# Performance work log

Hardware: AMD Instinct MI355X
Metric: run time of the kernel (lower is better)

## Reference

```python
import jax, jax.numpy as jnp
import numpy as np

# ---- configuration mirrored from init_kwargs ----
NUM_TREES = 8
NUM_NODES = 5
C = 16          # in_channels
B, H, W = 8, 224, 224
SEED = 0
NEG = -1e30     # maxplus semiring zero (avoid -inf for fp16/bf16 safety)


def make_forest():
    """Random recursive trees: node 0 is the root, parent[i] < i."""
    rng = np.random.default_rng(SEED)
    parents = []
    for _ in range(NUM_TREES):
        p = [-1] + [int(rng.integers(0, i)) for i in range(1, NUM_NODES)]
        parents.append(p)
    return parents


def excl_prefix_max(v):
    """Strict 2D prefix max: out[h,w] = max over h'<h, w'<w of v[h',w'].
    Semiring 'cumulative sum' (maxplus add = max) with exclusive shift."""
    c = jax.lax.cummax(jax.lax.cummax(v, axis=2), axis=3)
    c = c[:, :, :-1, :-1]
    return jnp.pad(c, ((0, 0), (0, 0), (1, 0), (1, 0)), constant_values=NEG)


def setup_inputs() -> dict:
    key = jax.random.key(0)
    kx, ka = jax.random.split(key)
    x = jax.random.normal(kx, (B, C, H, W), dtype=jnp.float32)
    alphas = jax.random.normal(ka, (NUM_TREES, NUM_NODES, C), dtype=jnp.float32)
    return {"x": x, "alphas": alphas}


def reference(x, alphas):
    parents = make_forest()  # static structure (seed-fixed)
    # valuate: map to log domain for the maxplus semiring
    xv = jnp.log1p(jax.nn.relu(x))  # [B, C, H, W]

    outs = []
    for t in range(NUM_TREES):
        par = parents[t]
        acc = [None] * NUM_NODES   # maxplus-product (= +) of children prefix maxes
        root_val = None
        # bottom-up over nodes (parent index < child index)
        for i in range(NUM_NODES - 1, -1, -1):
            # maxplus scaling by alpha: alpha + x
            v = xv + alphas[t, i][None, :, None, None]
            if acc[i] is not None:
                v = v + acc[i]          # semiring product with children
            if i > 0:
                s = excl_prefix_max(v)  # semiring cumulative over quadrant
                p = par[i]
                acc[p] = s if acc[p] is None else acc[p] + s
            else:
                root_val = v
        # root aggregation: maxplus sum over all pixels -> [B, C]
        outs.append(jnp.max(root_val, axis=(2, 3)))
    res = jnp.stack(outs, axis=1)  # [B, NUM_TREES, C]
    # devaluate: back from log domain
    return jnp.expm1(res)
```

## Files before the change

kernel.cpp:

```cpp
#include <hip/hip_runtime.h>
#include <stdint.h>

#define NTREES 8
#define NNODES 5
#define CC 16
#define BB 8
#define HH 224
#define WW 224
#define NBAND 56

struct Forest { int par[NTREES * NNODES]; };
struct Cls { int v[NTREES]; };

namespace nprng {

struct Pcg {
  __uint128_t state, inc;
  int has_uint32;
  uint32_t uinteger;
};

static inline __uint128_t pcg_mult() {
  return (((__uint128_t)0x2360ED051FC65DA4ULL) << 64) | 0x4385DF649FCCF645ULL;
}

static inline void pcg_step(Pcg& s) { s.state = s.state * pcg_mult() + s.inc; }

static inline uint64_t pcg_next64(Pcg& s) {
  pcg_step(s);
  uint64_t xored = (uint64_t)(s.state >> 64) ^ (uint64_t)s.state;
  unsigned rot = (unsigned)(s.state >> 122);
  return (xored >> rot) | (xored << ((64u - rot) & 63u));
}

static inline uint32_t pcg_next32(Pcg& s) {
  if (s.has_uint32) { s.has_uint32 = 0; return s.uinteger; }
  uint64_t n = pcg_next64(s);
  s.has_uint32 = 1;
  s.uinteger = (uint32_t)(n >> 32);
  return (uint32_t)n;
}

static inline uint32_t lemire32(Pcg& s, uint32_t rng) {
  const uint32_t rng_excl = rng + 1u;
  uint64_t m = (uint64_t)pcg_next32(s) * (uint64_t)rng_excl;
  uint32_t leftover = (uint32_t)m;
  if (leftover < rng_excl) {
    const uint32_t threshold = (uint32_t)((0xFFFFFFFFu - rng) % rng_excl);
    while (leftover < threshold) {
      m = (uint64_t)pcg_next32(s) * (uint64_t)rng_excl;
      leftover = (uint32_t)m;
    }
  }
  return (uint32_t)(m >> 32);
}

static void make_forest(Forest& f) {
  const uint32_t INIT_A = 0x43b0d7e5u, MULT_A = 0x931e8875u;
  const uint32_t INIT_B = 0x8b51f9ddu, MULT_B = 0x58f38dedu;
  const uint32_t MIX_L  = 0xca01f9ddu, MIX_R  = 0x4973f715u;
  uint32_t pool[4];
  uint32_t hc = INIT_A;
  auto hashmix = [&](uint32_t v) -> uint32_t {
    v ^= hc; hc *= MULT_A; v *= hc; v ^= v >> 16; return v;
  };
  auto mix = [&](uint32_t x, uint32_t y) -> uint32_t {
    uint32_t r = MIX_L * x - MIX_R * y; r ^= r >> 16; return r;
  };
  pool[0] = hashmix(0u);
  for (int i = 1; i < 4; ++i) pool[i] = hashmix(0u);
  for (int is = 0; is < 4; ++is)
    for (int id = 0; id < 4; ++id)
      if (is != id) pool[id] = mix(pool[id], hashmix(pool[is]));
  uint32_t st32[8];
  uint32_t hb = INIT_B;
  for (int i = 0; i < 8; ++i) {
    uint32_t dv = pool[i & 3];
    dv ^= hb; hb *= MULT_B; dv *= hb; dv ^= dv >> 16;
    st32[i] = dv;
  }
  uint64_t w64[4];
  for (int i = 0; i < 4; ++i)
    w64[i] = (uint64_t)st32[2 * i] | ((uint64_t)st32[2 * i + 1] << 32);

  __uint128_t initstate = (((__uint128_t)w64[0]) << 64) | w64[1];
  __uint128_t initseq   = (((__uint128_t)w64[2]) << 64) | w64[3];
  Pcg s;
  s.state = 0; s.inc = (initseq << 1) | 1;
  pcg_step(s);
  s.state += initstate;
  pcg_step(s);
  s.has_uint32 = 0; s.uinteger = 0;

  for (int t = 0; t < NTREES; ++t) {
    f.par[t * NNODES + 0] = -1;
    for (int i = 1; i < NNODES; ++i) {
      uint32_t rng = (uint32_t)(i - 1);
      f.par[t * NNODES + i] = (rng == 0) ? 0 : (int)lemire32(s, rng);
    }
  }
}

}

static int classify_tree(const int* p) {
  int nch[NNODES] = {0, 0, 0, 0, 0};
  for (int i = 1; i < NNODES; ++i) nch[p[i]]++;
  int internals[3], nI = 0;
  for (int i = 1; i <= 3; ++i) if (nch[i] > 0) internals[nI++] = i;
  if (nI == 0) return 1;
  if (nI == 1) {
    int m = nch[internals[0]];
    return m == 1 ? 2 : (m == 2 ? 3 : 4);
  }
  if (nI == 2) {
    int i = internals[0], j = internals[1];
    if (p[j] == i) {
      if (nch[j] == 2) return 9;
      return (nch[i] - 1 == 1) ? 7 : 6;
    }
    return 5;
  }
  return 8;
}

template <int CL> struct TC;
template <> struct TC<1> { static constexpr int H1=0,E1L=0,H2=0,E2L=0,H3=0,RL=4,R1=0,R2=0,R3=0; };
template <> struct TC<2> { static constexpr int H1=1,E1L=1,H2=0,E2L=0,H3=0,RL=2,R1=1,R2=0,R3=0; };
template <> struct TC<3> { static constexpr int H1=1,E1L=2,H2=0,E2L=0,H3=0,RL=1,R1=1,R2=0,R3=0; };
template <> struct TC<4> { static constexpr int H1=1,E1L=3,H2=0,E2L=0,H3=0,RL=0,R1=1,R2=0,R3=0; };
template <> struct TC<5> { static constexpr int H1=1,E1L=1,H2=0,E2L=0,H3=0,RL=0,R1=2,R2=0,R3=0; };
template <> struct TC<6> { static constexpr int H1=1,E1L=1,H2=1,E2L=0,H3=0,RL=1,R1=0,R2=1,R3=0; };
template <> struct TC<7> { static constexpr int H1=1,E1L=1,H2=1,E2L=1,H3=0,RL=0,R1=0,R2=1,R3=0; };
template <> struct TC<8> { static constexpr int H1=1,E1L=1,H2=1,E2L=0,H3=1,RL=0,R1=0,R2=0,R3=1; };
template <> struct TC<9> { static constexpr int H1=1,E1L=2,H2=1,E2L=0,H3=0,RL=0,R1=0,R2=1,R3=0; };

__device__ __forceinline__ float wshr1(float t) {
  int r = __builtin_amdgcn_update_dpp(
      0, __builtin_bit_cast(int, t), 0x138, 0xf, 0xf, true);
  return __builtin_bit_cast(float, r);
}

#define S4STAGE(MODS) \
  "v_max_f32_dpp %0, %0, %0 " MODS "\n\t" \
  "v_max_f32_dpp %1, %1, %1 " MODS "\n\t" \
  "v_max_f32_dpp %2, %2, %2 " MODS "\n\t" \
  "v_max_f32_dpp %3, %3, %3 " MODS "\n\t"

#define SCAN4(a, b, c, d)                                     \
  asm volatile(                                               \
      "s_nop 1\n\t"                                           \
      S4STAGE("row_shr:1 row_mask:0xf bank_mask:0xf")         \
      S4STAGE("row_shr:2 row_mask:0xf bank_mask:0xf")         \
      S4STAGE("row_shr:4 row_mask:0xf bank_mask:0xf")         \
      S4STAGE("row_shr:8 row_mask:0xf bank_mask:0xf")         \
      S4STAGE("row_bcast:15 row_mask:0xa bank_mask:0xf")      \
      S4STAGE("row_bcast:31 row_mask:0xc bank_mask:0xf")      \
      "s_nop 1"                                               \
      : "+v"(a), "+v"(b), "+v"(c), "+v"(d))

#define MUL4(d, s) { (d).x *= (s).x; (d).y *= (s).y; (d).z *= (s).z; (d).w *= (s).w; }
#define MAX4(d, s) { (d).x = fmaxf((d).x,(s).x); (d).y = fmaxf((d).y,(s).y); \
                     (d).z = fmaxf((d).z,(s).z); (d).w = fmaxf((d).w,(s).w); }

template <int E>
__device__ __forceinline__ void powmul(float4& v, const float4& s) {
  if constexpr (E == 4) {
    float4 t = s; MUL4(t, t); MUL4(t, t); MUL4(v, t);
  } else {
    if constexpr (E >= 1) MUL4(v, s);
    if constexpr (E >= 2) MUL4(v, s);
    if constexpr (E >= 3) MUL4(v, s);
  }
}

__device__ __forceinline__ void scan_pass(const float4 v[4], float4 S[4],
                                          const float4& carry) {
  float l1a = fmaxf(v[0].x, v[0].y), l2a = fmaxf(l1a, v[0].z), qa = fmaxf(l2a, v[0].w);
  float l1b = fmaxf(v[1].x, v[1].y), l2b = fmaxf(l1b, v[1].z), qb = fmaxf(l2b, v[1].w);
  float l1c = fmaxf(v[2].x, v[2].y), l2c = fmaxf(l1c, v[2].z), qc = fmaxf(l2c, v[2].w);
  float l1d = fmaxf(v[3].x, v[3].y), l2d = fmaxf(l1d, v[3].z), qd = fmaxf(l2d, v[3].w);
  SCAN4(qa, qb, qc, qd);
  float4 run = carry;
  {
    float e = wshr1(qa);
    run.x = fmaxf(run.x, e);
    run.y = fmaxf(run.y, fmaxf(e, v[0].x));
    run.z = fmaxf(run.z, fmaxf(e, l1a));
    run.w = fmaxf(run.w, fmaxf(e, l2a));
    S[0] = run;
  }
  {
    float e = wshr1(qb);
    run.x = fmaxf(run.x, e);
    run.y = fmaxf(run.y, fmaxf(e, v[1].x));
    run.z = fmaxf(run.z, fmaxf(e, l1b));
    run.w = fmaxf(run.w, fmaxf(e, l2b));
    S[1] = run;
  }
  {
    float e = wshr1(qc);
    run.x = fmaxf(run.x, e);
    run.y = fmaxf(run.y, fmaxf(e, v[2].x));
    run.z = fmaxf(run.z, fmaxf(e, l1c));
    run.w = fmaxf(run.w, fmaxf(e, l2c));
    S[2] = run;
  }
  {
    float e = wshr1(qd);
    run.x = fmaxf(run.x, e);
    run.y = fmaxf(run.y, fmaxf(e, v[3].x));
    run.z = fmaxf(run.z, fmaxf(e, l1d));
    run.w = fmaxf(run.w, fmaxf(e, l2d));
    S[3] = run;
  }
}

template <int CL>
__device__ __forceinline__ void run_tree(const float* __restrict__ cp,
                                         float mask, float asum,
                                         float* __restrict__ outp, int lane) {
  using F = TC<CL>;
  const float4 z4 = make_float4(0.f, 0.f, 0.f, 0.f);
  float4 cL = z4, c1 = z4, c2 = z4, c3 = z4, racc = z4;

  float4 X[4];
#pragma unroll
  for (int u = 0; u < 4; ++u) X[u] = *(const float4*)(cp + u * WW);

#pragma unroll 1
  for (int band = 0; band < NBAND; ++band) {
    const int nb = (band + 1 < NBAND) ? band + 1 : NBAND - 1;
    float4 T[4];
#pragma unroll
    for (int u = 0; u < 4; ++u)
      T[u] = *(const float4*)(cp + (size_t)(nb * 4 + u) * WW);

    float4 fv[4];
#pragma unroll
    for (int u = 0; u < 4; ++u) {
      const float4 xr = X[u];
      fv[u].x = fmaf(fmaxf(xr.x, 0.f), mask, mask);
      fv[u].y = fmaf(fmaxf(xr.y, 0.f), mask, mask);
      fv[u].z = fmaf(fmaxf(xr.z, 0.f), mask, mask);
      fv[u].w = fmaf(fmaxf(xr.w, 0.f), mask, mask);
    }

    float4 SL[4], S1[4], S2[4], S3[4];

    scan_pass(fv, SL, cL);

    if constexpr (F::H1) {
      float4 v[4];
#pragma unroll
      for (int u = 0; u < 4; ++u) {
        v[u] = fv[u];
        powmul<F::E1L>(v[u], (u == 0) ? cL : SL[u - 1]);
      }
      scan_pass(v, S1, c1);
    }

    if constexpr (F::H2) {
      float4 v[4];
#pragma unroll
      for (int u = 0; u < 4; ++u) {
        v[u] = fv[u];
        if constexpr (F::E2L > 0) powmul<F::E2L>(v[u], (u == 0) ? cL : SL[u - 1]);
        { float4 s = (u == 0) ? c1 : S1[u - 1]; MUL4(v[u], s); }
      }
      scan_pass(v, S2, c2);
    }

    if constexpr (F::H3) {
      float4 v[4];
#pragma unroll
      for (int u = 0; u < 4; ++u) {
        v[u] = fv[u];
        { float4 s = (u == 0) ? c2 : S2[u - 1]; MUL4(v[u], s); }
      }
      scan_pass(v, S3, c3);
    }

#pragma unroll
    for (int u = 0; u < 4; ++u) {
      float4 r = fv[u];
      if constexpr (F::RL > 0) powmul<F::RL>(r, (u == 0) ? cL : SL[u - 1]);
      if constexpr (F::R1 > 0) powmul<F::R1>(r, (u == 0) ? c1 : S1[u - 1]);
      if constexpr (F::R2 > 0) powmul<F::R2>(r, (u == 0) ? c2 : S2[u - 1]);
      if constexpr (F::R3 > 0) powmul<F::R3>(r, (u == 0) ? c3 : S3[u - 1]);
      MAX4(racc, r);
    }

    cL = SL[3];
    if constexpr (F::H1) c1 = S1[3];
    if constexpr (F::H2) c2 = S2[3];
    if constexpr (F::H3) c3 = S3[3];

#pragma unroll
    for (int u = 0; u < 4; ++u) X[u] = T[u];
  }

  float m = fmaxf(fmaxf(racc.x, racc.y), fmaxf(racc.z, racc.w));
#pragma unroll
  for (int d = 1; d < 64; d <<= 1) m = fmaxf(m, __shfl_xor(m, d));
  if (lane == 0) *outp = expf(asum) * m - 1.f;
}

__global__ __launch_bounds__(64) void fis_kernel(const float* __restrict__ x,
                                                 const float* __restrict__ alphas,
                                                 float* __restrict__ out,
                                                 Cls cls) {
  const int lane = threadIdx.x;
  const int blk  = blockIdx.x;
  const int t    = blk >> 7;
  const int bc   = blk & 127;
  const int c    = bc & (CC - 1);
  const int b    = bc >> 4;

  const float* __restrict__ xp = x + (size_t)bc * (HH * WW);

  float asum = 0.f;
#pragma unroll
  for (int i = 0; i < NNODES; ++i) asum += alphas[(t * NNODES + i) * CC + c];

  const int   w0   = lane * 4;
  const float mask = (w0 < WW) ? 1.0f : 0.0f;
  const float* __restrict__ cp = xp + ((w0 < WW) ? w0 : (WW - 4));
  float* outp = out + ((size_t)b * NTREES + t) * CC + c;

  switch (cls.v[t]) {
    case 1: run_tree<1>(cp, mask, asum, outp, lane); break;
    case 2: run_tree<2>(cp, mask, asum, outp, lane); break;
    case 3: run_tree<3>(cp, mask, asum, outp, lane); break;
    case 4: run_tree<4>(cp, mask, asum, outp, lane); break;
    case 5: run_tree<5>(cp, mask, asum, outp, lane); break;
    case 6: run_tree<6>(cp, mask, asum, outp, lane); break;
    case 7: run_tree<7>(cp, mask, asum, outp, lane); break;
    case 8: run_tree<8>(cp, mask, asum, outp, lane); break;
    case 9: run_tree<9>(cp, mask, asum, outp, lane); break;
    default: break;
  }
}

extern "C" void kernel_launch(void* const* d_in, const int* in_sizes, int n_in,
                              void* d_out, int out_size, void* d_ws, size_t ws_size,
                              hipStream_t stream) {
  const float* x      = (const float*)d_in[0];
  const float* alphas = (const float*)d_in[1];
  float* out          = (float*)d_out;

  Forest f;
  nprng::make_forest(f);

  Cls cls;
  for (int t = 0; t < NTREES; ++t)
    cls.v[t] = classify_tree(&f.par[t * NNODES]);

  dim3 grid(BB * CC * NTREES);
  dim3 block(64);
  hipLaunchKernelGGL(fis_kernel, grid, block, 0, stream, x, alphas, out, cls);
}
```

Baseline: 100.3 us.

## Software-pipeline tree depth levels across bands to batch DPP scans

Restructures the per-band loop so each tree depth level works on a band lagged by one per level. All level scans then go into a single batched DPP asm block of up to 16 independent chains instead of several dependent 4-wide scans. This is meant to hide DPP latency and cut s_nop and serialization overhead per band. In exchange it keeps more live registers (delayed fv copies, previous-band scan state) and runs a few extra drain iterations with a zeroed mask.

```diff
diff --git a/kernel.cpp b/kernel.cpp
--- a/kernel.cpp
+++ b/kernel.cpp
@@ -141,23 +141,34 @@
   return __builtin_bit_cast(float, r);
 }
 
-#define S4STAGE(MODS) \
-  "v_max_f32_dpp %0, %0, %0 " MODS "\n\t" \
-  "v_max_f32_dpp %1, %1, %1 " MODS "\n\t" \
-  "v_max_f32_dpp %2, %2, %2 " MODS "\n\t" \
-  "v_max_f32_dpp %3, %3, %3 " MODS "\n\t"
-
-#define SCAN4(a, b, c, d)                                     \
-  asm volatile(                                               \
-      "s_nop 1\n\t"                                           \
-      S4STAGE("row_shr:1 row_mask:0xf bank_mask:0xf")         \
-      S4STAGE("row_shr:2 row_mask:0xf bank_mask:0xf")         \
-      S4STAGE("row_shr:4 row_mask:0xf bank_mask:0xf")         \
-      S4STAGE("row_shr:8 row_mask:0xf bank_mask:0xf")         \
-      S4STAGE("row_bcast:15 row_mask:0xa bank_mask:0xf")      \
-      S4STAGE("row_bcast:31 row_mask:0xc bank_mask:0xf")      \
-      "s_nop 1"                                               \
-      : "+v"(a), "+v"(b), "+v"(c), "+v"(d))
+#define DPP_S1  "row_shr:1 row_mask:0xf bank_mask:0xf"
+#define DPP_S2  "row_shr:2 row_mask:0xf bank_mask:0xf"
+#define DPP_S4  "row_shr:4 row_mask:0xf bank_mask:0xf"
+#define DPP_S8  "row_shr:8 row_mask:0xf bank_mask:0xf"
+#define DPP_B15 "row_bcast:15 row_mask:0xa bank_mask:0xf"
+#define DPP_B31 "row_bcast:31 row_mask:0xc bank_mask:0xf"
+
+#define OPROW(n, M) "v_max_f32_dpp %" #n ", %" #n ", %" #n " " M "\n\t"
+
+#define OPS4(M)  OPROW(0,M) OPROW(1,M) OPROW(2,M) OPROW(3,M)
+#define OPS8(M)  OPS4(M)  OPROW(4,M) OPROW(5,M) OPROW(6,M) OPROW(7,M)
+#define OPS12(M) OPS8(M)  OPROW(8,M) OPROW(9,M) OPROW(10,M) OPROW(11,M)
+#define OPS16(M) OPS12(M) OPROW(12,M) OPROW(13,M) OPROW(14,M) OPROW(15,M)
+
+#define SCANBODY(OPS) \
+  "s_nop 1\n\t" OPS(DPP_S1) OPS(DPP_S2) OPS(DPP_S4) OPS(DPP_S8) \
+  OPS(DPP_B15) OPS(DPP_B31) "s_nop 1"
+
+#define SCAN4Q(q)  asm volatile(SCANBODY(OPS4)  : "+v"((q)[0]), "+v"((q)[1]), "+v"((q)[2]), "+v"((q)[3]))
+#define SCAN8Q(q)  asm volatile(SCANBODY(OPS8)  : "+v"((q)[0]), "+v"((q)[1]), "+v"((q)[2]), "+v"((q)[3]), \
+                                                  "+v"((q)[4]), "+v"((q)[5]), "+v"((q)[6]), "+v"((q)[7]))
+#define SCAN12Q(q) asm volatile(SCANBODY(OPS12) : "+v"((q)[0]), "+v"((q)[1]), "+v"((q)[2]), "+v"((q)[3]), \
+                                                  "+v"((q)[4]), "+v"((q)[5]), "+v"((q)[6]), "+v"((q)[7]), \
+                                                  "+v"((q)[8]), "+v"((q)[9]), "+v"((q)[10]), "+v"((q)[11]))
+#define SCAN16Q(q) asm volatile(SCANBODY(OPS16) : "+v"((q)[0]), "+v"((q)[1]), "+v"((q)[2]), "+v"((q)[3]), \
+                                                  "+v"((q)[4]), "+v"((q)[5]), "+v"((q)[6]), "+v"((q)[7]), \
+                                                  "+v"((q)[8]), "+v"((q)[9]), "+v"((q)[10]), "+v"((q)[11]), \
+                                                  "+v"((q)[12]), "+v"((q)[13]), "+v"((q)[14]), "+v"((q)[15]))
 
 #define MUL4(d, s) { (d).x *= (s).x; (d).y *= (s).y; (d).z *= (s).z; (d).w *= (s).w; }
 #define MAX4(d, s) { (d).x = fmaxf((d).x,(s).x); (d).y = fmaxf((d).y,(s).y); \
@@ -174,45 +185,34 @@
   }
 }
 
-__device__ __forceinline__ void scan_pass(const float4 v[4], float4 S[4],
-                                          const float4& carry) {
-  float l1a = fmaxf(v[0].x, v[0].y), l2a = fmaxf(l1a, v[0].z), qa = fmaxf(l2a, v[0].w);
-  float l1b = fmaxf(v[1].x, v[1].y), l2b = fmaxf(l1b, v[1].z), qb = fmaxf(l2b, v[1].w);
-  float l1c = fmaxf(v[2].x, v[2].y), l2c = fmaxf(l1c, v[2].z), qc = fmaxf(l2c, v[2].w);
-  float l1d = fmaxf(v[3].x, v[3].y), l2d = fmaxf(l1d, v[3].z), qd = fmaxf(l2d, v[3].w);
-  SCAN4(qa, qb, qc, qd);
-  float4 run = carry;
-  {
-    float e = wshr1(qa);
+__device__ __forceinline__ float4 srcat(const float4 S[4], const float4& tail, int u) {
+  return (u == 0) ? tail : S[u - 1];
+}
+
+struct LocB { float x0[4], l1[4], l2[4]; };
+
+__device__ __forceinline__ void mk_q(const float4 v[4], LocB& L, float* q) {
+#pragma unroll
+  for (int u = 0; u < 4; ++u) {
+    L.x0[u] = v[u].x;
+    L.l1[u] = fmaxf(v[u].x, v[u].y);
+    L.l2[u] = fmaxf(L.l1[u], v[u].z);
+    q[u]    = fmaxf(L.l2[u], v[u].w);
+  }
+}
+
+__device__ __forceinline__ void run_update(const LocB& L, const float* q,
+                                           float4 S[4], float4& tail) {
+  tail = S[3];
+  float4 run = tail;
+#pragma unroll
+  for (int u = 0; u < 4; ++u) {
+    float e = wshr1(q[u]);
     run.x = fmaxf(run.x, e);
-    run.y = fmaxf(run.y, fmaxf(e, v[0].x));
-    run.z = fmaxf(run.z, fmaxf(e, l1a));
-    run.w = fmaxf(run.w, fmaxf(e, l2a));
-    S[0] = run;
-  }
-  {
-    float e = wshr1(qb);
-    run.x = fmaxf(run.x, e);
-    run.y = fmaxf(run.y, fmaxf(e, v[1].x));
-    run.z = fmaxf(run.z, fmaxf(e, l1b));
-    run.w = fmaxf(run.w, fmaxf(e, l2b));
-    S[1] = run;
-  }
-  {
-    float e = wshr1(qc);
-    run.x = fmaxf(run.x, e);
-    run.y = fmaxf(run.y, fmaxf(e, v[2].x));
-    run.z = fmaxf(run.z, fmaxf(e, l1c));
-    run.w = fmaxf(run.w, fmaxf(e, l2c));
-    S[2] = run;
-  }
-  {
-    float e = wshr1(qd);
-    run.x = fmaxf(run.x, e);
-    run.y = fmaxf(run.y, fmaxf(e, v[3].x));
-    run.z = fmaxf(run.z, fmaxf(e, l1d));
-    run.w = fmaxf(run.w, fmaxf(e, l2d));
-    S[3] = run;
+    run.y = fmaxf(run.y, fmaxf(e, L.x0[u]));
+    run.z = fmaxf(run.z, fmaxf(e, L.l1[u]));
+    run.w = fmaxf(run.w, fmaxf(e, L.l2[u]));
+    S[u] = run;
   }
 }
 
@@ -221,81 +221,129 @@
                                          float mask, float asum,
                                          float* __restrict__ outp, int lane) {
   using F = TC<CL>;
+  constexpr int D = 1 + F::H1 + F::H2 + F::H3;
+  constexpr bool NEEDM1 = (F::H2 != 0) && (F::E2L > 0 || F::RL > 0);
   const float4 z4 = make_float4(0.f, 0.f, 0.f, 0.f);
-  float4 cL = z4, c1 = z4, c2 = z4, c3 = z4, racc = z4;
+
+  float4 SL[4] = {z4, z4, z4, z4}, S1[4] = {z4, z4, z4, z4};
+  float4 S2[4] = {z4, z4, z4, z4}, S3[4] = {z4, z4, z4, z4};
+  float4 SLm1[4] = {z4, z4, z4, z4};
+  float4 tailL = z4, tail1 = z4, tail2 = z4, tail3 = z4, tailLm1 = z4;
+  float4 fv1[4] = {z4, z4, z4, z4}, fv2[4] = {z4, z4, z4, z4},
+         fv3[4] = {z4, z4, z4, z4};
+  float4 racc = z4;
 
   float4 X[4];
 #pragma unroll
   for (int u = 0; u < 4; ++u) X[u] = *(const float4*)(cp + u * WW);
 
 #pragma unroll 1
-  for (int band = 0; band < NBAND; ++band) {
-    const int nb = (band + 1 < NBAND) ? band + 1 : NBAND - 1;
+  for (int i = 0; i < NBAND + D - 1; ++i) {
+    const int nb = (i + 1 < NBAND) ? (i + 1) : (NBAND - 1);
     float4 T[4];
 #pragma unroll
     for (int u = 0; u < 4; ++u)
       T[u] = *(const float4*)(cp + (size_t)(nb * 4 + u) * WW);
 
-    float4 fv[4];
+    const float bm = (i < NBAND) ? mask : 0.f;
+    float4 fv0[4];
 #pragma unroll
     for (int u = 0; u < 4; ++u) {
-      const float4 xr = X[u];
-      fv[u].x = fmaf(fmaxf(xr.x, 0.f), mask, mask);
-      fv[u].y = fmaf(fmaxf(xr.y, 0.f), mask, mask);
-      fv[u].z = fmaf(fmaxf(xr.z, 0.f), mask, mask);
-      fv[u].w = fmaf(fmaxf(xr.w, 0.f), mask, mask);
-    }
-
-    float4 SL[4], S1[4], S2[4], S3[4];
-
-    scan_pass(fv, SL, cL);
-
+      fv0[u].x = fmaf(fmaxf(X[u].x, 0.f), bm, bm);
+      fv0[u].y = fmaf(fmaxf(X[u].y, 0.f), bm, bm);
+      fv0[u].z = fmaf(fmaxf(X[u].z, 0.f), bm, bm);
+      fv0[u].w = fmaf(fmaxf(X[u].w, 0.f), bm, bm);
+    }
+
+    LocB loL, lo1, lo2, lo3;
+    float q[16];
+    mk_q(fv0, loL, q + 0);
     if constexpr (F::H1) {
       float4 v[4];
 #pragma unroll
       for (int u = 0; u < 4; ++u) {
-        v[u] = fv[u];
-        powmul<F::E1L>(v[u], (u == 0) ? cL : SL[u - 1]);
+        v[u] = fv1[u];
+        powmul<F::E1L>(v[u], srcat(SL, tailL, u));
       }
-      scan_pass(v, S1, c1);
-    }
-
+      mk_q(v, lo1, q + 4);
+    }
     if constexpr (F::H2) {
       float4 v[4];
 #pragma unroll
       for (int u = 0; u < 4; ++u) {
-        v[u] = fv[u];
-        if constexpr (F::E2L > 0) powmul<F::E2L>(v[u], (u == 0) ? cL : SL[u - 1]);
-        { float4 s = (u == 0) ? c1 : S1[u - 1]; MUL4(v[u], s); }
+        v[u] = fv2[u];
+        if constexpr (F::E2L > 0) powmul<F::E2L>(v[u], srcat(SLm1, tailLm1, u));
+        float4 s = srcat(S1, tail1, u);
+        MUL4(v[u], s);
       }
-      scan_pass(v, S2, c2);
-    }
-
+      mk_q(v, lo2, q + 8);
+    }
     if constexpr (F::H3) {
       float4 v[4];
 #pragma unroll
       for (int u = 0; u < 4; ++u) {
-        v[u] = fv[u];
-        { float4 s = (u == 0) ? c2 : S2[u - 1]; MUL4(v[u], s); }
+        v[u] = fv3[u];
+        float4 s = srcat(S2, tail2, u);
+        MUL4(v[u], s);
       }
-      scan_pass(v, S3, c3);
-    }
-
-#pragma unroll
-    for (int u = 0; u < 4; ++u) {
-      float4 r = fv[u];
-      if constexpr (F::RL > 0) powmul<F::RL>(r, (u == 0) ? cL : SL[u - 1]);
-      if constexpr (F::R1 > 0) powmul<F::R1>(r, (u == 0) ? c1 : S1[u - 1]);
-      if constexpr (F::R2 > 0) powmul<F::R2>(r, (u == 0) ? c2 : S2[u - 1]);
-      if constexpr (F::R3 > 0) powmul<F::R3>(r, (u == 0) ? c3 : S3[u - 1]);
-      MAX4(racc, r);
-    }
-
-    cL = SL[3];
-    if constexpr (F::H1) c1 = S1[3];
-    if constexpr (F::H2) c2 = S2[3];
-    if constexpr (F::H3) c3 = S3[3];
-
+      mk_q(v, lo3, q + 12);
+    }
+
+    if constexpr (D == 1)      { SCAN4Q(q); }
+    else if constexpr (D == 2) { SCAN8Q(q); }
+    else if constexpr (D == 3) { SCAN12Q(q); }
+    else                       { SCAN16Q(q); }
+
+    if constexpr (F::H3) run_update(lo3, q + 12, S3, tail3);
+    if constexpr (F::H2) run_update(lo2, q + 8, S2, tail2);
+    if constexpr (F::H1) run_update(lo1, q + 4, S1, tail1);
+
+    if constexpr (D > 1) {
+#pragma unroll
+      for (int u = 0; u < 4; ++u) {
+        float4 r;
+        if constexpr (D == 2) r = fv1[u];
+        else if constexpr (D == 3) r = fv2[u];
+        else r = fv3[u];
+        if constexpr (F::RL > 0) {
+          if constexpr (D == 2) powmul<F::RL>(r, srcat(SL, tailL, u));
+          else                  powmul<F::RL>(r, srcat(SLm1, tailLm1, u));
+        }
+        if constexpr (F::R1 > 0) powmul<F::R1>(r, srcat(S1, tail1, u));
+        if constexpr (F::R2 > 0) powmul<F::R2>(r, srcat(S2, tail2, u));
+        if constexpr (F::R3 > 0) powmul<F::R3>(r, srcat(S3, tail3, u));
+        MAX4(racc, r);
+      }
+    }
+
+    if constexpr (NEEDM1) {
+#pragma unroll
+      for (int u = 0; u < 4; ++u) SLm1[u] = SL[u];
+      tailLm1 = tailL;
+    }
+    run_update(loL, q + 0, SL, tailL);
+
+    if constexpr (D == 1) {
+#pragma unroll
+      for (int u = 0; u < 4; ++u) {
+        float4 r = fv0[u];
+        powmul<F::RL>(r, srcat(SL, tailL, u));
+        MAX4(racc, r);
+      }
+    }
+
+    if constexpr (D >= 4) {
+#pragma unroll
+      for (int u = 0; u < 4; ++u) fv3[u] = fv2[u];
+    }
+    if constexpr (D >= 3) {
+#pragma unroll
+      for (int u = 0; u < 4; ++u) fv2[u] = fv1[u];
+    }
+    if constexpr (D >= 2) {
+#pragma unroll
+      for (int u = 0; u < 4; ++u) fv1[u] = fv0[u];
+    }
 #pragma unroll
     for (int u = 0; u < 4; ++u) X[u] = T[u];
   }
```

After: 107.1 us. 6.7% more time.
